# Kernel optimization log

Measured on AMD Instinct MI355X. Metric: run time of the kernel, lower is better.

Reference implementation:

```python
import jax, jax.numpy as jnp
import numpy as np

T2I = {'START': 0, 'STOP': 1, 'O': 2, 'B_nr': 3, 'M_nr': 4, 'E_nr': 5,
       'B_ns': 6, 'M_ns': 7, 'E_ns': 8, 'B_nt': 9, 'M_nt': 10, 'E_nt': 11}
START, STOP = T2I['START'], T2I['STOP']
NT = 12            # tag_size
B, T = 32, 256     # batch, seq_len
V, E = 100000, 256 # vocab, embedding_dim
H = 256            # hidden_dim // 2 (per direction)
NEG = -10000.0


def _masked_transitions():
    # replicate init_transitions() exactly on a randn matrix
    rng = np.random.default_rng(0)
    tr = rng.standard_normal((NT, NT)).astype(np.float32)
    t = T2I
    tr[t['START'], :] = NEG
    tr[:, t['STOP']] = NEG
    tag_list = ['nr', 'ns', 'nt']
    for tag in tag_list:
        tr[t['O'], t['M_' + tag]] = NEG
        tr[t['O'], t['B_' + tag]] = NEG
        tr[t['STOP'], t['M_' + tag]] = NEG
        tr[t['STOP'], t['B_' + tag]] = NEG
    for to in tag_list:
        for fr in tag_list:
            tr[t['B_' + to], t['B_' + fr]] = NEG
            tr[t['B_' + to], t['M_' + fr]] = NEG
    for to in tag_list:
        tr[t['M_' + to], t['O']] = NEG
        tr[t['M_' + to], t['START']] = NEG
        tr[t['M_' + to], t['E_' + to]] = NEG
        for fr in tag_list:
            if fr == to:
                continue
            tr[t['M_' + to], t['B_' + fr]] = NEG
            tr[t['M_' + to], t['M_' + fr]] = NEG
            tr[t['M_' + to], t['E_' + fr]] = NEG
    for to in tag_list:
        tr[t['E_' + to], t['O']] = NEG
        tr[t['E_' + to], t['START']] = NEG
        tr[t['E_' + to], t['E_' + to]] = NEG
        for fr in tag_list:
            if fr == to:
                continue
            tr[t['E_' + to], t['B_' + fr]] = NEG
            tr[t['E_' + to], t['M_' + fr]] = NEG
            tr[t['E_' + to], t['E_' + fr]] = NEG
    return jnp.asarray(tr)


def setup_inputs() -> dict:
    key = jax.random.key(0)
    ks = jax.random.split(key, 16)
    s = 1.0 / np.sqrt(H)
    return {
        'sentences': jax.random.randint(ks[0], (B, T), 0, V),
        'tags': jax.random.randint(ks[1], (B, T), 2, NT),  # non-special tags
        'lengths': jnp.full((B,), T, dtype=jnp.int32),
        'embedding': jax.random.normal(ks[2], (V, E), jnp.float32),
        'W_ih_f': jax.random.uniform(ks[3], (4 * H, E), jnp.float32, -s, s),
        'W_hh_f': jax.random.uniform(ks[4], (4 * H, H), jnp.float32, -s, s),
        'b_ih_f': jax.random.uniform(ks[5], (4 * H,), jnp.float32, -s, s),
        'b_hh_f': jax.random.uniform(ks[6], (4 * H,), jnp.float32, -s, s),
        'W_ih_b': jax.random.uniform(ks[7], (4 * H, E), jnp.float32, -s, s),
        'W_hh_b': jax.random.uniform(ks[8], (4 * H, H), jnp.float32, -s, s),
        'b_ih_b': jax.random.uniform(ks[9], (4 * H,), jnp.float32, -s, s),
        'b_hh_b': jax.random.uniform(ks[10], (4 * H,), jnp.float32, -s, s),
        'W_out': jax.random.uniform(ks[11], (NT, 2 * H), jnp.float32, -s, s),
        'b_out': jax.random.uniform(ks[12], (NT,), jnp.float32, -s, s),
        'transitions': _masked_transitions(),
        'h0': jax.random.normal(ks[13], (2, B, H), jnp.float32),
        'c0': jax.random.normal(ks[14], (2, B, H), jnp.float32),
    }


def _lstm_dir(x, W_ih, W_hh, b_ih, b_hh, h0, c0, reverse):
    # x: [B, T, E]; PyTorch gate order i, f, g, o
    xs = jnp.swapaxes(x, 0, 1)  # [T, B, E]
    if reverse:
        xs = xs[::-1]
    def step(carry, xt):
        h, c = carry
        g = xt @ W_ih.T + b_ih + h @ W_hh.T + b_hh  # [B, 4H]
        i, f, gg, o = jnp.split(g, 4, axis=-1)
        c = jax.nn.sigmoid(f) * c + jax.nn.sigmoid(i) * jnp.tanh(gg)
        h = jax.nn.sigmoid(o) * jnp.tanh(c)
        return (h, c), h
    _, hs = jax.lax.scan(step, (h0, c0), xs)
    if reverse:
        hs = hs[::-1]
    return jnp.swapaxes(hs, 0, 1)  # [B, T, H]


def _crf_log_z(feats, trans):
    # feats: [T, NT] — log-domain forward algorithm (exact _forward_alg math)
    init = jnp.full((NT,), NEG, dtype=feats.dtype).at[START].set(0.0)
    def step(fv, feat):
        # next[i] = logsumexp_j(fv[j] + feat[i] + trans[i, j])
        return jax.nn.logsumexp(fv[None, :] + feat[:, None] + trans, axis=1), None
    fv, _ = jax.lax.scan(step, init, feats)
    return jax.nn.logsumexp(fv + trans[STOP])


def _gold_score(feats, tag, trans):
    # feats: [T, NT], tag: [T]
    prev = jnp.concatenate([jnp.array([START], dtype=tag.dtype), tag[:-1]])
    em = jnp.take_along_axis(feats, tag[:, None], axis=1).sum()
    tr = trans[tag, prev].sum() + trans[STOP, tag[-1]]
    return em + tr


def reference(sentences, tags, lengths, embedding, W_ih_f, W_hh_f, b_ih_f, b_hh_f,
              W_ih_b, W_hh_b, b_ih_b, b_hh_b, W_out, b_out, transitions, h0, c0):
    # neg_log_likelihood path (lengths are all == T, so feats[:length] is full)
    emb = embedding[sentences]  # [B, T, E] gather (memory-bound)
    fwd = _lstm_dir(emb, W_ih_f, W_hh_f, b_ih_f, b_hh_f, h0[0], c0[0], False)
    bwd = _lstm_dir(emb, W_ih_b, W_hh_b, b_ih_b, b_hh_b, h0[1], c0[1], True)
    feats = jnp.concatenate([fwd, bwd], axis=-1) @ W_out.T + b_out  # [B, T, NT]
    forward_score = jax.vmap(_crf_log_z, in_axes=(0, None))(feats, transitions).sum()
    gold_score = jax.vmap(_gold_score, in_axes=(0, 0, None))(feats, tags, transitions).sum()
    return forward_score - gold_score
```

## Files before the change

### kernel.cpp

```cpp
#include <hip/hip_runtime.h>
#include <hip/hip_bf16.h>

typedef unsigned int u32;
typedef unsigned short u16;
typedef unsigned char u8;

typedef __attribute__((ext_vector_type(4))) float f32x4;
typedef __attribute__((ext_vector_type(8))) int i32x8;
typedef __attribute__((ext_vector_type(8))) __bf16 bf16x8;

#define NEG (-10000.0f)
#define WSCALE 16.0f

__device__ __forceinline__ float bf2f(u16 x){ return __uint_as_float(((u32)x) << 16); }
__device__ __forceinline__ u16 f2bf(float f){
    u32 u = __float_as_uint(f);
    u32 r = (u + 0x7fffu + ((u >> 16) & 1u)) >> 16;
    return (u16)r;
}
__device__ __forceinline__ u32 pk_bf16(float lo, float hi){
    u32 r;
    asm volatile("v_cvt_pk_bf16_f32 %0, %1, %2" : "=v"(r) : "v"(lo), "v"(hi));
    return r;
}
__device__ __forceinline__ float hsig1(float a){
    return __builtin_amdgcn_fmed3f(a, 0.0f, 1.0f);
}
__device__ __forceinline__ float ptanh(float x){
    return x * __builtin_amdgcn_rsqf(__builtin_fmaf(x, x, 1.0f));
}

__global__ void k0_convert(const float* __restrict__ Whh_f,
                           const float* __restrict__ Whh_b,
                           const float* __restrict__ Wout,
                           u32* __restrict__ w8, u32* __restrict__ w8o){
    int gid = blockIdx.x * blockDim.x + threadIdx.x;
    if (gid >= 131072) return;
    int idx = gid * 4;
    int dir = idx >> 18;
    int off = idx & 0x3FFFF;
    const float* W = dir ? Whh_b : Whh_f;
    int pk = __builtin_amdgcn_cvt_pk_fp8_f32(W[off] * WSCALE, W[off + 1] * WSCALE, 0, false);
    pk = __builtin_amdgcn_cvt_pk_fp8_f32(W[off + 2] * WSCALE, W[off + 3] * WSCALE, pk, true);
    w8[gid] = (u32)pk;

    if (gid < 2048){
        int i4 = gid * 4;
        int n = i4 >> 9, k = i4 & 511;
        float a = 0, b = 0, c = 0, d = 0;
        if (n < 12){
            const float* wr = Wout + (size_t)n * 512 + k;
            a = wr[0] * 64.0f; b = wr[1] * 64.0f; c = wr[2] * 64.0f; d = wr[3] * 64.0f;
        }
        int p = __builtin_amdgcn_cvt_pk_fp8_f32(a, b, 0, false);
        p = __builtin_amdgcn_cvt_pk_fp8_f32(c, d, p, true);
        w8o[gid] = (u32)p;
    }
}

__global__ __launch_bounds__(256) void k1_inproj(
    const int* __restrict__ sent, const float* __restrict__ emb,
    const float* __restrict__ Wih_f, const float* __restrict__ bih_f, const float* __restrict__ bhh_f,
    const float* __restrict__ Wih_b, const float* __restrict__ bih_b, const float* __restrict__ bhh_b,
    u16* __restrict__ X){
    int dir = blockIdx.z;
    const float* W  = dir ? Wih_b : Wih_f;
    const float* b1 = dir ? bih_b : bih_f;
    const float* b2 = dir ? bhh_b : bhh_f;
    u16* Xo = X + (size_t)dir * 8388608;

    __shared__ __align__(16) u16 As[64 * 256];
    __shared__ __align__(16) u16 Bs[64 * 256];

    int tid = threadIdx.x;
    int m0 = blockIdx.x * 64, n0 = blockIdx.y * 64;

    {
        int r = tid >> 2, q = tid & 3;
        int sid = sent[m0 + r];
        const float* arow = emb + (size_t)sid * 256 + q * 64;
        const float* brow = W + (size_t)(n0 + r) * 256 + q * 64;
        #pragma unroll
        for (int g = 0; g < 8; g++){
            int col8 = q * 8 + g;
            int sc = col8 ^ (r & 7);
            float4 a0 = *(const float4*)(arow + g * 8);
            float4 a1 = *(const float4*)(arow + g * 8 + 4);
            u32 pa[4] = { pk_bf16(a0.x, a0.y), pk_bf16(a0.z, a0.w),
                          pk_bf16(a1.x, a1.y), pk_bf16(a1.z, a1.w) };
            *(uint4*)&As[r * 256 + sc * 8] = *(uint4*)pa;
            float4 v0 = *(const float4*)(brow + g * 8);
            float4 v1 = *(const float4*)(brow + g * 8 + 4);
            u32 pb[4] = { pk_bf16(v0.x, v0.y), pk_bf16(v0.z, v0.w),
                          pk_bf16(v1.x, v1.y), pk_bf16(v1.z, v1.w) };
            *(uint4*)&Bs[r * 256 + sc * 8] = *(uint4*)pb;
        }
    }
    __syncthreads();

    int w = tid >> 6, l = tid & 63, lr = l & 15, lk = l >> 4;

    f32x4 acc[4];
    #pragma unroll
    for (int nt = 0; nt < 4; nt++) acc[nt] = (f32x4){0.f, 0.f, 0.f, 0.f};

    int am = w * 16 + lr;
    #pragma unroll
    for (int ko = 0; ko < 8; ko++){
        bf16x8 a = *(const bf16x8*)&As[am * 256 + ((ko * 4 + lk) ^ (am & 7)) * 8];
        #pragma unroll
        for (int nt = 0; nt < 4; nt++){
            int bn = nt * 16 + lr;
            bf16x8 bb = *(const bf16x8*)&Bs[bn * 256 + ((ko * 4 + lk) ^ (bn & 7)) * 8];
            acc[nt] = __builtin_amdgcn_mfma_f32_16x16x32_bf16(a, bb, acc[nt], 0, 0, 0);
        }
    }

    #pragma unroll
    for (int nt = 0; nt < 4; nt++){
        int n = n0 + nt * 16 + lr;
        float bias = b1[n] + b2[n];
        int gate = n >> 8, hid = n & 255;
        int pos = (hid >> 1) * 8 + gate * 2 + (hid & 1);
        bool sig = (gate != 2);
        #pragma unroll
        for (int reg = 0; reg < 4; reg++){
            int m = m0 + w * 16 + lk * 4 + reg;
            float v = acc[nt][reg] + bias;
            if (sig) v = __builtin_fmaf(0.25f, v, 0.5f);
            Xo[(size_t)m * 1024 + pos] = f2bf(v);
        }
    }
}

#define GSCALE(g2) ((g2) == 2 ? 0x7B7B7B7B : 0x79797979)

#define K2_STEP(S, XC, XN)                                                        \
{                                                                                 \
    int tt = dir ? (255 - (S)) : (S);                                             \
    int cur = (S) & 1, nxt = cur ^ 1;                                             \
    int sn = ((S) + 1 < 256) ? (S) + 1 : (S);                                     \
    int tn = dir ? (255 - sn) : sn;                                               \
    const u8* xband = xbase + (u32)(tn * 2048);                                   \
    _Pragma("unroll")                                                             \
    for (int r2 = 0; r2 < 4; r2++)                                                \
        XN[r2] = *(const uint4*)(xband + xo[r2]);                                 \
    i32x8 af0 = *(const i32x8*)&hl[cur][lr][lk * 32];                             \
    i32x8 af1 = *(const i32x8*)&hl[cur][lr][128 + lk * 32];                       \
    f32x4 acc0[4], acc1[4];                                                       \
    _Pragma("unroll")                                                             \
    for (int g2 = 0; g2 < 4; g2++){                                               \
        u32 w0 = ((const u32*)&XC[0])[g2];                                        \
        u32 w1 = ((const u32*)&XC[1])[g2];                                        \
        u32 w2 = ((const u32*)&XC[2])[g2];                                        \
        u32 w3 = ((const u32*)&XC[3])[g2];                                        \
        acc0[g2] = (f32x4){ __uint_as_float(w0 << 16),                            \
                            __uint_as_float(w1 << 16),                            \
                            __uint_as_float(w2 << 16),                            \
                            __uint_as_float(w3 << 16) };                          \
        acc1[g2] = (f32x4){ __uint_as_float(w0 & 0xFFFF0000u),                    \
                            __uint_as_float(w1 & 0xFFFF0000u),                    \
                            __uint_as_float(w2 & 0xFFFF0000u),                    \
                            __uint_as_float(w3 & 0xFFFF0000u) };                  \
    }                                                                             \
    __builtin_amdgcn_s_setprio(1);                                                \
    _Pragma("unroll")                                                             \
    for (int g2 = 0; g2 < 4; g2++){                                               \
        acc0[g2] = __builtin_amdgcn_mfma_scale_f32_16x16x128_f8f6f4(              \
            af0, wf[g2][0][0], acc0[g2], 0, 0, 0, 0x7F7F7F7F, 0, GSCALE(g2));     \
        acc0[g2] = __builtin_amdgcn_mfma_scale_f32_16x16x128_f8f6f4(              \
            af1, wf[g2][0][1], acc0[g2], 0, 0, 0, 0x7F7F7F7F, 0, GSCALE(g2));     \
    }                                                                             \
    _Pragma("unroll")                                                             \
    for (int g2 = 0; g2 < 4; g2++){                                               \
        acc1[g2] = __builtin_amdgcn_mfma_scale_f32_16x16x128_f8f6f4(              \
            af0, wf[g2][1][0], acc1[g2], 0, 0, 0, 0x7F7F7F7F, 0, GSCALE(g2));     \
        acc1[g2] = __builtin_amdgcn_mfma_scale_f32_16x16x128_f8f6f4(              \
            af1, wf[g2][1][1], acc1[g2], 0, 0, 0, 0x7F7F7F7F, 0, GSCALE(g2));     \
    }                                                                             \
    __builtin_amdgcn_s_setprio(0);                                                \
    float hh0v[4];                                                                \
    _Pragma("unroll")                                                             \
    for (int r2 = 0; r2 < 4; r2++){                                               \
        float gi = hsig1(acc0[0][r2]);                                            \
        float gf = hsig1(acc0[1][r2]);                                            \
        float gg = ptanh(acc0[2][r2]);                                            \
        float go = hsig1(acc0[3][r2]);                                            \
        cst[0][r2] = gf * cst[0][r2] + gi * gg;                                   \
        hh0v[r2] = go * ptanh(cst[0][r2]);                                        \
    }                                                                             \
    u8* hband = hbase + (u32)(tt * 256);                                          \
    _Pragma("unroll")                                                             \
    for (int r2 = 0; r2 < 4; r2++){                                               \
        float gi = hsig1(acc1[0][r2]);                                            \
        float gf = hsig1(acc1[1][r2]);                                            \
        float gg = ptanh(acc1[2][r2]);                                            \
        float go = hsig1(acc1[3][r2]);                                            \
        cst[1][r2] = gf * cst[1][r2] + gi * gg;                                   \
        float hh1 = go * ptanh(cst[1][r2]);                                       \
        int pk = __builtin_amdgcn_cvt_pk_fp8_f32(hh0v[r2], hh1, 0, false);        \
        *(u16*)&hl[nxt][lk * 4 + r2][hid0] = (u16)pk;                             \
        *(u16*)(hband + ho[r2]) = (u16)pk;                                        \
    }                                                                             \
    asm volatile("s_waitcnt lgkmcnt(0)" ::: "memory");                            \
    __builtin_amdgcn_s_barrier();                                                 \
    __builtin_amdgcn_sched_barrier(0);                                            \
}

__global__ __launch_bounds__(512) void k2_lstm(
    const u16* __restrict__ X, const u8* __restrict__ w8,
    const float* __restrict__ h0, const float* __restrict__ c0,
    u8* __restrict__ HS8){

    int wg = blockIdx.x;
    int dir = wg >> 1, half = wg & 1;
    int tid = threadIdx.x;
    int w = tid >> 6, l = tid & 63;
    int lr = l & 15, lk = l >> 4;
    int bbase = half * 16;

    __shared__ __align__(16) u8 hl[2][16][272];

    const u8* Wd = w8 + (size_t)dir * 262144;

    int hid0 = w * 32 + 2 * lr;
    int hp = w * 16 + lr;

    i32x8 wf[4][2][2];
    #pragma unroll
    for (int g = 0; g < 4; g++)
        #pragma unroll
        for (int t = 0; t < 2; t++)
            #pragma unroll
            for (int ko = 0; ko < 2; ko++)
                wf[g][t][ko] = *(const i32x8*)(Wd + (size_t)(g * 256 + hid0 + t) * 256
                                               + ko * 128 + lk * 32);

    float cst[2][4];
    #pragma unroll
    for (int t = 0; t < 2; t++)
        #pragma unroll
        for (int r = 0; r < 4; r++)
            cst[t][r] = c0[(size_t)(dir * 32 + bbase + lk * 4 + r) * 256 + hid0 + t];

    const u8* xbase = (const u8*)(X + (size_t)dir * 8388608);
    u8* hbase = HS8 + (size_t)dir * 2097152;
    u32 xo[4], ho[4];
    #pragma unroll
    for (int r = 0; r < 4; r++){
        xo[r] = (u32)((bbase + lk * 4 + r) * 524288 + hp * 16);
        ho[r] = (u32)((bbase + lk * 4 + r) * 65536 + hid0);
    }

    {
        int row = tid >> 5;
        int col = (tid & 31) * 8;
        const float* src = h0 + (size_t)(dir * 32 + bbase + row) * 256 + col;
        int p0 = __builtin_amdgcn_cvt_pk_fp8_f32(src[0], src[1], 0, false);
        p0 = __builtin_amdgcn_cvt_pk_fp8_f32(src[2], src[3], p0, true);
        int p1 = __builtin_amdgcn_cvt_pk_fp8_f32(src[4], src[5], 0, false);
        p1 = __builtin_amdgcn_cvt_pk_fp8_f32(src[6], src[7], p1, true);
        u32* dst = (u32*)&hl[0][row][col];
        dst[0] = (u32)p0; dst[1] = (u32)p1;
    }
    __syncthreads();

    uint4 xpA[4], xpB[4];
    {
        int tt0 = dir ? 255 : 0;
        const u8* xband = xbase + (u32)(tt0 * 2048);
        #pragma unroll
        for (int r = 0; r < 4; r++)
            xpA[r] = *(const uint4*)(xband + xo[r]);
    }

    for (int s2 = 0; s2 < 256; s2 += 2){
        K2_STEP(s2,     xpA, xpB);
        K2_STEP(s2 + 1, xpB, xpA);
    }
}

__global__ __launch_bounds__(256) void k3_feats(
    const u8* __restrict__ HS8, const u8* __restrict__ W8o,
    const float* __restrict__ bout, float* __restrict__ feats){
    int tid = threadIdx.x;
    int wv = tid >> 6, l = tid & 63, lr = l & 15, lk = l >> 4;
    int tile = blockIdx.x * 4 + wv;
    int b = tile >> 4, t0 = (tile & 15) * 16;

    const u8* hf = HS8 + (size_t)b * 65536 + (t0 + lr) * 256;
    const u8* hb = HS8 + (size_t)(32 + b) * 65536 + (t0 + lr) * 256;
    const u8* wo = W8o + lr * 512;

    f32x4 acc = (f32x4){0.f, 0.f, 0.f, 0.f};
    #pragma unroll
    for (int ko = 0; ko < 8; ko++){
        long a = *(const long*)(hf + ko * 32 + lk * 8);
        long bb = *(const long*)(wo + ko * 32 + lk * 8);
        acc = __builtin_amdgcn_mfma_f32_16x16x32_fp8_fp8(a, bb, acc, 0, 0, 0);
    }
    #pragma unroll
    for (int ko = 0; ko < 8; ko++){
        long a = *(const long*)(hb + ko * 32 + lk * 8);
        long bb = *(const long*)(wo + 256 + ko * 32 + lk * 8);
        acc = __builtin_amdgcn_mfma_f32_16x16x32_fp8_fp8(a, bb, acc, 0, 0, 0);
    }

    if (lr < 12){
        float bias = bout[lr];
        #pragma unroll
        for (int reg = 0; reg < 4; reg++){
            int t = t0 + lk * 4 + reg;
            feats[((size_t)b * 256 + t) * 12 + lr] = acc[reg] * 0.015625f + bias;
        }
    }
}

__global__ __launch_bounds__(64) void k4_crf(
    const float* __restrict__ feats, const float* __restrict__ trans,
    const int* __restrict__ tags, float* __restrict__ scores){
    int b = blockIdx.x;
    int l = threadIdx.x;
    int i = l >> 2, q = l & 3;
    bool act = (i < 12);
    int j0 = q * 3;
    float tj0 = act ? trans[i * 12 + j0 + 0] : NEG;
    float tj1 = act ? trans[i * 12 + j0 + 1] : NEG;
    float tj2 = act ? trans[i * 12 + j0 + 2] : NEG;
    float fv0 = (j0 == 0) ? 0.0f : NEG;
    float fv1 = NEG, fv2 = NEG;
    const float* fb = feats + (size_t)b * 3072;
    float fcur = act ? fb[i] : 0.0f;

    for (int t = 0; t < 256; t++){
        float e0, e1, e2;
        if (act){ e0 = fv0 + tj0; e1 = fv1 + tj1; e2 = fv2 + tj2; }
        else    { e0 = e1 = e2 = NEG; }
        float m3 = fmaxf(fmaxf(e0, e1), e2);
        m3 = fmaxf(m3, __shfl_xor(m3, 1, 4));
        m3 = fmaxf(m3, __shfl_xor(m3, 2, 4));
        float s = __expf(e0 - m3) + __expf(e1 - m3) + __expf(e2 - m3);
        s += __shfl_xor(s, 1, 4);
        s += __shfl_xor(s, 2, 4);
        float fvnew = fcur + m3 + __logf(s);
        if (t < 255) fcur = act ? fb[(t + 1) * 12 + i] : 0.0f;
        fv0 = __shfl(fvnew, (j0 + 0) * 4 + q);
        fv1 = __shfl(fvnew, (j0 + 1) * 4 + q);
        fv2 = __shfl(fvnew, (j0 + 2) * 4 + q);
    }

    float e0 = fv0 + trans[12 + j0 + 0];
    float e1 = fv1 + trans[12 + j0 + 1];
    float e2 = fv2 + trans[12 + j0 + 2];
    float m3 = fmaxf(fmaxf(e0, e1), e2);
    m3 = fmaxf(m3, __shfl_xor(m3, 1, 4));
    m3 = fmaxf(m3, __shfl_xor(m3, 2, 4));
    float s = __expf(e0 - m3) + __expf(e1 - m3) + __expf(e2 - m3);
    s += __shfl_xor(s, 1, 4);
    s += __shfl_xor(s, 2, 4);
    float logZ = m3 + __logf(s);

    const int* tg = tags + b * 256;
    float g = 0.0f;
    for (int t = l; t < 256; t += 64){
        int cur = tg[t];
        int prev = t ? tg[t - 1] : 0;
        g += fb[t * 12 + cur] + trans[cur * 12 + prev];
    }
    #pragma unroll
    for (int off = 32; off; off >>= 1) g += __shfl_xor(g, off, 64);
    if (l == 0) scores[b] = logZ - (g + trans[12 + tg[255]]);
}

__global__ void k5_final(const float* __restrict__ scores, float* __restrict__ out){
    int t = threadIdx.x;
    float v = scores[t];
    #pragma unroll
    for (int off = 16; off; off >>= 1) v += __shfl_xor(v, off, 32);
    if (t == 0) out[0] = v;
}

extern "C" void kernel_launch(void* const* d_in, const int* in_sizes, int n_in,
                              void* d_out, int out_size, void* d_ws, size_t ws_size,
                              hipStream_t stream){
    const int*   sent  = (const int*)d_in[0];
    const int*   tags  = (const int*)d_in[1];
    const float* emb   = (const float*)d_in[3];
    const float* Wih_f = (const float*)d_in[4];
    const float* Whh_f = (const float*)d_in[5];
    const float* bih_f = (const float*)d_in[6];
    const float* bhh_f = (const float*)d_in[7];
    const float* Wih_b = (const float*)d_in[8];
    const float* Whh_b = (const float*)d_in[9];
    const float* bih_b = (const float*)d_in[10];
    const float* bhh_b = (const float*)d_in[11];
    const float* Wout  = (const float*)d_in[12];
    const float* bout  = (const float*)d_in[13];
    const float* trans = (const float*)d_in[14];
    const float* h0    = (const float*)d_in[15];
    const float* c0    = (const float*)d_in[16];

    char* ws = (char*)d_ws;
    u16*   X      = (u16*)(ws);
    u8*    HS8    = (u8*)(ws + 33554432);
    float* FEATS  = (float*)(ws + 41943040);
    u8*    W8     = (u8*)(ws + 42336256);
    float* SCORES = (float*)(ws + 43384832);
    u8*    W8o    = (u8*)(ws + 43384960);

    hipLaunchKernelGGL(k0_convert, dim3(512), dim3(256), 0, stream,
                       Whh_f, Whh_b, Wout, (u32*)W8, (u32*)W8o);
    hipLaunchKernelGGL(k1_inproj, dim3(128, 16, 2), dim3(256), 0, stream,
                       sent, emb, Wih_f, bih_f, bhh_f, Wih_b, bih_b, bhh_b, X);
    hipLaunchKernelGGL(k2_lstm, dim3(4), dim3(512), 0, stream, X, W8, h0, c0, HS8);
    hipLaunchKernelGGL(k3_feats, dim3(128), dim3(256), 0, stream, HS8, W8o, bout, FEATS);
    hipLaunchKernelGGL(k4_crf, dim3(32), dim3(64), 0, stream, FEATS, trans, tags, SCORES);
    hipLaunchKernelGGL(k5_final, dim3(1), dim3(32), 0, stream, SCORES, (float*)d_out);
}
```

Baseline: 446.5 us.

## Double LSTM recurrence block to 1024 threads, one hidden unit per lane

```diff
diff --git a/kernel.cpp b/kernel.cpp
--- a/kernel.cpp
+++ b/kernel.cpp
@@ -121,7 +121,7 @@
         int n = n0 + nt * 16 + lr;
         float bias = b1[n] + b2[n];
         int gate = n >> 8, hid = n & 255;
-        int pos = (hid >> 1) * 8 + gate * 2 + (hid & 1);
+        int pos = hid * 4 + gate;
         bool sig = (gate != 2);
         #pragma unroll
         for (int reg = 0; reg < 4; reg++){
@@ -144,70 +144,46 @@
     const u8* xband = xbase + (u32)(tn * 2048);                                   \
     _Pragma("unroll")                                                             \
     for (int r2 = 0; r2 < 4; r2++)                                                \
-        XN[r2] = *(const uint4*)(xband + xo[r2]);                                 \
+        XN[r2] = *(const uint2*)(xband + xo[r2]);                                 \
     i32x8 af0 = *(const i32x8*)&hl[cur][lr][lk * 32];                             \
     i32x8 af1 = *(const i32x8*)&hl[cur][lr][128 + lk * 32];                       \
-    f32x4 acc0[4], acc1[4];                                                       \
+    f32x4 acc[4];                                                                 \
     _Pragma("unroll")                                                             \
-    for (int g2 = 0; g2 < 4; g2++){                                               \
-        u32 w0 = ((const u32*)&XC[0])[g2];                                        \
-        u32 w1 = ((const u32*)&XC[1])[g2];                                        \
-        u32 w2 = ((const u32*)&XC[2])[g2];                                        \
-        u32 w3 = ((const u32*)&XC[3])[g2];                                        \
-        acc0[g2] = (f32x4){ __uint_as_float(w0 << 16),                            \
-                            __uint_as_float(w1 << 16),                            \
-                            __uint_as_float(w2 << 16),                            \
-                            __uint_as_float(w3 << 16) };                          \
-        acc1[g2] = (f32x4){ __uint_as_float(w0 & 0xFFFF0000u),                    \
-                            __uint_as_float(w1 & 0xFFFF0000u),                    \
-                            __uint_as_float(w2 & 0xFFFF0000u),                    \
-                            __uint_as_float(w3 & 0xFFFF0000u) };                  \
+    for (int r2 = 0; r2 < 4; r2++){                                               \
+        u32 w0 = XC[r2].x, w1 = XC[r2].y;                                         \
+        acc[0][r2] = __uint_as_float(w0 << 16);                                   \
+        acc[1][r2] = __uint_as_float(w0 & 0xFFFF0000u);                           \
+        acc[2][r2] = __uint_as_float(w1 << 16);                                   \
+        acc[3][r2] = __uint_as_float(w1 & 0xFFFF0000u);                           \
     }                                                                             \
     __builtin_amdgcn_s_setprio(1);                                                \
     _Pragma("unroll")                                                             \
     for (int g2 = 0; g2 < 4; g2++){                                               \
-        acc0[g2] = __builtin_amdgcn_mfma_scale_f32_16x16x128_f8f6f4(              \
-            af0, wf[g2][0][0], acc0[g2], 0, 0, 0, 0x7F7F7F7F, 0, GSCALE(g2));     \
-        acc0[g2] = __builtin_amdgcn_mfma_scale_f32_16x16x128_f8f6f4(              \
-            af1, wf[g2][0][1], acc0[g2], 0, 0, 0, 0x7F7F7F7F, 0, GSCALE(g2));     \
-    }                                                                             \
-    _Pragma("unroll")                                                             \
-    for (int g2 = 0; g2 < 4; g2++){                                               \
-        acc1[g2] = __builtin_amdgcn_mfma_scale_f32_16x16x128_f8f6f4(              \
-            af0, wf[g2][1][0], acc1[g2], 0, 0, 0, 0x7F7F7F7F, 0, GSCALE(g2));     \
-        acc1[g2] = __builtin_amdgcn_mfma_scale_f32_16x16x128_f8f6f4(              \
-            af1, wf[g2][1][1], acc1[g2], 0, 0, 0, 0x7F7F7F7F, 0, GSCALE(g2));     \
+        acc[g2] = __builtin_amdgcn_mfma_scale_f32_16x16x128_f8f6f4(               \
+            af0, wf[g2][0], acc[g2], 0, 0, 0, 0x7F7F7F7F, 0, GSCALE(g2));         \
+        acc[g2] = __builtin_amdgcn_mfma_scale_f32_16x16x128_f8f6f4(               \
+            af1, wf[g2][1], acc[g2], 0, 0, 0, 0x7F7F7F7F, 0, GSCALE(g2));         \
     }                                                                             \
     __builtin_amdgcn_s_setprio(0);                                                \
-    float hh0v[4];                                                                \
-    _Pragma("unroll")                                                             \
-    for (int r2 = 0; r2 < 4; r2++){                                               \
-        float gi = hsig1(acc0[0][r2]);                                            \
-        float gf = hsig1(acc0[1][r2]);                                            \
-        float gg = ptanh(acc0[2][r2]);                                            \
-        float go = hsig1(acc0[3][r2]);                                            \
-        cst[0][r2] = gf * cst[0][r2] + gi * gg;                                   \
-        hh0v[r2] = go * ptanh(cst[0][r2]);                                        \
-    }                                                                             \
     u8* hband = hbase + (u32)(tt * 256);                                          \
     _Pragma("unroll")                                                             \
     for (int r2 = 0; r2 < 4; r2++){                                               \
-        float gi = hsig1(acc1[0][r2]);                                            \
-        float gf = hsig1(acc1[1][r2]);                                            \
-        float gg = ptanh(acc1[2][r2]);                                            \
-        float go = hsig1(acc1[3][r2]);                                            \
-        cst[1][r2] = gf * cst[1][r2] + gi * gg;                                   \
-        float hh1 = go * ptanh(cst[1][r2]);                                       \
-        int pk = __builtin_amdgcn_cvt_pk_fp8_f32(hh0v[r2], hh1, 0, false);        \
-        *(u16*)&hl[nxt][lk * 4 + r2][hid0] = (u16)pk;                             \
-        *(u16*)(hband + ho[r2]) = (u16)pk;                                        \
+        float gi = hsig1(acc[0][r2]);                                             \
+        float gf = hsig1(acc[1][r2]);                                             \
+        float gg = ptanh(acc[2][r2]);                                             \
+        float go = hsig1(acc[3][r2]);                                             \
+        cst[r2] = gf * cst[r2] + gi * gg;                                         \
+        float hh = go * ptanh(cst[r2]);                                           \
+        int pk = __builtin_amdgcn_cvt_pk_fp8_f32(hh, hh, 0, false);               \
+        hl[nxt][lk * 4 + r2][hid] = (u8)pk;                                       \
+        *(hband + ho[r2]) = (u8)pk;                                               \
     }                                                                             \
     asm volatile("s_waitcnt lgkmcnt(0)" ::: "memory");                            \
     __builtin_amdgcn_s_barrier();                                                 \
     __builtin_amdgcn_sched_barrier(0);                                            \
 }
 
-__global__ __launch_bounds__(512) void k2_lstm(
+__global__ __launch_bounds__(1024) void k2_lstm(
     const u16* __restrict__ X, const u8* __restrict__ w8,
     const float* __restrict__ h0, const float* __restrict__ c0,
     u8* __restrict__ HS8){
@@ -223,55 +199,47 @@
 
     const u8* Wd = w8 + (size_t)dir * 262144;
 
-    int hid0 = w * 32 + 2 * lr;
-    int hp = w * 16 + lr;
-
-    i32x8 wf[4][2][2];
+    int hid = w * 16 + lr;
+
+    i32x8 wf[4][2];
     #pragma unroll
     for (int g = 0; g < 4; g++)
         #pragma unroll
-        for (int t = 0; t < 2; t++)
-            #pragma unroll
-            for (int ko = 0; ko < 2; ko++)
-                wf[g][t][ko] = *(const i32x8*)(Wd + (size_t)(g * 256 + hid0 + t) * 256
-                                               + ko * 128 + lk * 32);
-
-    float cst[2][4];
-    #pragma unroll
-    for (int t = 0; t < 2; t++)
-        #pragma unroll
-        for (int r = 0; r < 4; r++)
-            cst[t][r] = c0[(size_t)(dir * 32 + bbase + lk * 4 + r) * 256 + hid0 + t];
+        for (int ko = 0; ko < 2; ko++)
+            wf[g][ko] = *(const i32x8*)(Wd + (size_t)(g * 256 + hid) * 256
+                                        + ko * 128 + lk * 32);
+
+    float cst[4];
+    #pragma unroll
+    for (int r = 0; r < 4; r++)
+        cst[r] = c0[(size_t)(dir * 32 + bbase + lk * 4 + r) * 256 + hid];
 
     const u8* xbase = (const u8*)(X + (size_t)dir * 8388608);
     u8* hbase = HS8 + (size_t)dir * 2097152;
     u32 xo[4], ho[4];
     #pragma unroll
     for (int r = 0; r < 4; r++){
-        xo[r] = (u32)((bbase + lk * 4 + r) * 524288 + hp * 16);
-        ho[r] = (u32)((bbase + lk * 4 + r) * 65536 + hid0);
+        xo[r] = (u32)((bbase + lk * 4 + r) * 524288 + hid * 8);
+        ho[r] = (u32)((bbase + lk * 4 + r) * 65536 + hid);
     }
 
     {
-        int row = tid >> 5;
-        int col = (tid & 31) * 8;
+        int row = tid >> 6;
+        int col = (tid & 63) * 4;
         const float* src = h0 + (size_t)(dir * 32 + bbase + row) * 256 + col;
         int p0 = __builtin_amdgcn_cvt_pk_fp8_f32(src[0], src[1], 0, false);
         p0 = __builtin_amdgcn_cvt_pk_fp8_f32(src[2], src[3], p0, true);
-        int p1 = __builtin_amdgcn_cvt_pk_fp8_f32(src[4], src[5], 0, false);
-        p1 = __builtin_amdgcn_cvt_pk_fp8_f32(src[6], src[7], p1, true);
-        u32* dst = (u32*)&hl[0][row][col];
-        dst[0] = (u32)p0; dst[1] = (u32)p1;
+        *(u32*)&hl[0][row][col] = (u32)p0;
     }
     __syncthreads();
 
-    uint4 xpA[4], xpB[4];
+    uint2 xpA[4], xpB[4];
     {
         int tt0 = dir ? 255 : 0;
         const u8* xband = xbase + (u32)(tt0 * 2048);
         #pragma unroll
         for (int r = 0; r < 4; r++)
-            xpA[r] = *(const uint4*)(xband + xo[r]);
+            xpA[r] = *(const uint2*)(xband + xo[r]);
     }
 
     for (int s2 = 0; s2 < 256; s2 += 2){
@@ -412,7 +380,7 @@
                        Whh_f, Whh_b, Wout, (u32*)W8, (u32*)W8o);
     hipLaunchKernelGGL(k1_inproj, dim3(128, 16, 2), dim3(256), 0, stream,
                        sent, emb, Wih_f, bih_f, bhh_f, Wih_b, bih_b, bhh_b, X);
-    hipLaunchKernelGGL(k2_lstm, dim3(4), dim3(512), 0, stream, X, W8, h0, c0, HS8);
+    hipLaunchKernelGGL(k2_lstm, dim3(4), dim3(1024), 0, stream, X, W8, h0, c0, HS8);
     hipLaunchKernelGGL(k3_feats, dim3(128), dim3(256), 0, stream, HS8, W8o, bout, FEATS);
     hipLaunchKernelGGL(k4_crf, dim3(32), dim3(64), 0, stream, FEATS, trans, tags, SCORES);
     hipLaunchKernelGGL(k5_final, dim3(1), dim3(32), 0, stream, SCORES, (float*)d_out);
```

Result: slower. 1.022 ms (+128.9%).

## Reuse gathered embedding tile across N blocks and fold final reduction into atomics

Applied to the files above, without the earlier changes.

```diff
diff --git a/kernel.cpp b/kernel.cpp
--- a/kernel.cpp
+++ b/kernel.cpp
@@ -33,8 +33,10 @@
 __global__ void k0_convert(const float* __restrict__ Whh_f,
                            const float* __restrict__ Whh_b,
                            const float* __restrict__ Wout,
-                           u32* __restrict__ w8, u32* __restrict__ w8o){
+                           u32* __restrict__ w8, u32* __restrict__ w8o,
+                           float* __restrict__ out){
     int gid = blockIdx.x * blockDim.x + threadIdx.x;
+    if (gid == 0) out[0] = 0.0f;
     if (gid >= 131072) return;
     int idx = gid * 4;
     int dir = idx >> 18;
@@ -73,62 +75,77 @@
     __shared__ __align__(16) u16 Bs[64 * 256];
 
     int tid = threadIdx.x;
-    int m0 = blockIdx.x * 64, n0 = blockIdx.y * 64;
+    int m0 = blockIdx.x * 64;
+    int ntbase = blockIdx.y * 8;
+
+    int sr = tid >> 2, sq = tid & 3;
 
     {
-        int r = tid >> 2, q = tid & 3;
-        int sid = sent[m0 + r];
-        const float* arow = emb + (size_t)sid * 256 + q * 64;
-        const float* brow = W + (size_t)(n0 + r) * 256 + q * 64;
+        int sid = sent[m0 + sr];
+        const float* arow = emb + (size_t)sid * 256 + sq * 64;
         #pragma unroll
         for (int g = 0; g < 8; g++){
-            int col8 = q * 8 + g;
-            int sc = col8 ^ (r & 7);
+            int col8 = sq * 8 + g;
+            int sc = col8 ^ (sr & 7);
             float4 a0 = *(const float4*)(arow + g * 8);
             float4 a1 = *(const float4*)(arow + g * 8 + 4);
             u32 pa[4] = { pk_bf16(a0.x, a0.y), pk_bf16(a0.z, a0.w),
                           pk_bf16(a1.x, a1.y), pk_bf16(a1.z, a1.w) };
-            *(uint4*)&As[r * 256 + sc * 8] = *(uint4*)pa;
-            float4 v0 = *(const float4*)(brow + g * 8);
-            float4 v1 = *(const float4*)(brow + g * 8 + 4);
-            u32 pb[4] = { pk_bf16(v0.x, v0.y), pk_bf16(v0.z, v0.w),
-                          pk_bf16(v1.x, v1.y), pk_bf16(v1.z, v1.w) };
-            *(uint4*)&Bs[r * 256 + sc * 8] = *(uint4*)pb;
-        }
-    }
-    __syncthreads();
+            *(uint4*)&As[sr * 256 + sc * 8] = *(uint4*)pa;
+        }
+    }
 
     int w = tid >> 6, l = tid & 63, lr = l & 15, lk = l >> 4;
-
-    f32x4 acc[4];
-    #pragma unroll
-    for (int nt = 0; nt < 4; nt++) acc[nt] = (f32x4){0.f, 0.f, 0.f, 0.f};
-
     int am = w * 16 + lr;
-    #pragma unroll
-    for (int ko = 0; ko < 8; ko++){
-        bf16x8 a = *(const bf16x8*)&As[am * 256 + ((ko * 4 + lk) ^ (am & 7)) * 8];
+
+    for (int nb = 0; nb < 8; nb++){
+        int n0 = (ntbase + nb) * 64;
+
+        __syncthreads();
+        {
+            const float* brow = W + (size_t)(n0 + sr) * 256 + sq * 64;
+            #pragma unroll
+            for (int g = 0; g < 8; g++){
+                int col8 = sq * 8 + g;
+                int sc = col8 ^ (sr & 7);
+                float4 v0 = *(const float4*)(brow + g * 8);
+                float4 v1 = *(const float4*)(brow + g * 8 + 4);
+                u32 pb[4] = { pk_bf16(v0.x, v0.y), pk_bf16(v0.z, v0.w),
+                              pk_bf16(v1.x, v1.y), pk_bf16(v1.z, v1.w) };
+                *(uint4*)&Bs[sr * 256 + sc * 8] = *(uint4*)pb;
+            }
+        }
+        __syncthreads();
+
+        f32x4 acc[4];
+        #pragma unroll
+        for (int nt = 0; nt < 4; nt++) acc[nt] = (f32x4){0.f, 0.f, 0.f, 0.f};
+
+        #pragma unroll
+        for (int ko = 0; ko < 8; ko++){
+            bf16x8 a = *(const bf16x8*)&As[am * 256 + ((ko * 4 + lk) ^ (am & 7)) * 8];
+            #pragma unroll
+            for (int nt = 0; nt < 4; nt++){
+                int bn = nt * 16 + lr;
+                bf16x8 bb = *(const bf16x8*)&Bs[bn * 256 + ((ko * 4 + lk) ^ (bn & 7)) * 8];
+                acc[nt] = __builtin_amdgcn_mfma_f32_16x16x32_bf16(a, bb, acc[nt], 0, 0, 0);
+            }
+        }
+
         #pragma unroll
         for (int nt = 0; nt < 4; nt++){
-            int bn = nt * 16 + lr;
-            bf16x8 bb = *(const bf16x8*)&Bs[bn * 256 + ((ko * 4 + lk) ^ (bn & 7)) * 8];
-            acc[nt] = __builtin_amdgcn_mfma_f32_16x16x32_bf16(a, bb, acc[nt], 0, 0, 0);
-        }
-    }
-
-    #pragma unroll
-    for (int nt = 0; nt < 4; nt++){
-        int n = n0 + nt * 16 + lr;
-        float bias = b1[n] + b2[n];
-        int gate = n >> 8, hid = n & 255;
-        int pos = (hid >> 1) * 8 + gate * 2 + (hid & 1);
-        bool sig = (gate != 2);
-        #pragma unroll
-        for (int reg = 0; reg < 4; reg++){
-            int m = m0 + w * 16 + lk * 4 + reg;
-            float v = acc[nt][reg] + bias;
-            if (sig) v = __builtin_fmaf(0.25f, v, 0.5f);
-            Xo[(size_t)m * 1024 + pos] = f2bf(v);
+            int n = n0 + nt * 16 + lr;
+            float bias = b1[n] + b2[n];
+            int gate = n >> 8, hid = n & 255;
+            int pos = (hid >> 1) * 8 + gate * 2 + (hid & 1);
+            bool sig = (gate != 2);
+            #pragma unroll
+            for (int reg = 0; reg < 4; reg++){
+                int m = m0 + w * 16 + lk * 4 + reg;
+                float v = acc[nt][reg] + bias;
+                if (sig) v = __builtin_fmaf(0.25f, v, 0.5f);
+                Xo[(size_t)m * 1024 + pos] = f2bf(v);
+            }
         }
     }
 }
@@ -318,7 +335,7 @@
 
 __global__ __launch_bounds__(64) void k4_crf(
     const float* __restrict__ feats, const float* __restrict__ trans,
-    const int* __restrict__ tags, float* __restrict__ scores){
+    const int* __restrict__ tags, float* __restrict__ out){
     int b = blockIdx.x;
     int l = threadIdx.x;
     int i = l >> 2, q = l & 3;
@@ -369,15 +386,7 @@
     }
     #pragma unroll
     for (int off = 32; off; off >>= 1) g += __shfl_xor(g, off, 64);
-    if (l == 0) scores[b] = logZ - (g + trans[12 + tg[255]]);
-}
-
-__global__ void k5_final(const float* __restrict__ scores, float* __restrict__ out){
-    int t = threadIdx.x;
-    float v = scores[t];
-    #pragma unroll
-    for (int off = 16; off; off >>= 1) v += __shfl_xor(v, off, 32);
-    if (t == 0) out[0] = v;
+    if (l == 0) atomicAdd(out, logZ - (g + trans[12 + tg[255]]));
 }
 
 extern "C" void kernel_launch(void* const* d_in, const int* in_sizes, int n_in,
@@ -405,15 +414,13 @@
     u8*    HS8    = (u8*)(ws + 33554432);
     float* FEATS  = (float*)(ws + 41943040);
     u8*    W8     = (u8*)(ws + 42336256);
-    float* SCORES = (float*)(ws + 43384832);
     u8*    W8o    = (u8*)(ws + 43384960);
 
     hipLaunchKernelGGL(k0_convert, dim3(512), dim3(256), 0, stream,
-                       Whh_f, Whh_b, Wout, (u32*)W8, (u32*)W8o);
-    hipLaunchKernelGGL(k1_inproj, dim3(128, 16, 2), dim3(256), 0, stream,
+                       Whh_f, Whh_b, Wout, (u32*)W8, (u32*)W8o, (float*)d_out);
+    hipLaunchKernelGGL(k1_inproj, dim3(128, 2, 2), dim3(256), 0, stream,
                        sent, emb, Wih_f, bih_f, bhh_f, Wih_b, bih_b, bhh_b, X);
     hipLaunchKernelGGL(k2_lstm, dim3(4), dim3(512), 0, stream, X, W8, h0, c0, HS8);
     hipLaunchKernelGGL(k3_feats, dim3(128), dim3(256), 0, stream, HS8, W8o, bout, FEATS);
-    hipLaunchKernelGGL(k4_crf, dim3(32), dim3(64), 0, stream, FEATS, trans, tags, SCORES);
-    hipLaunchKernelGGL(k5_final, dim3(1), dim3(32), 0, stream, SCORES, (float*)d_out);
-}
+    hipLaunchKernelGGL(k4_crf, dim3(32), dim3(64), 0, stream, FEATS, trans, tags, (float*)d_out);
+}
```

After: 412.0 us (median of 2 runs). 1.08x faster.
